# Kernel optimization log

Hardware: AMD Instinct MI355X
Metric: run time of the kernel (lower is better)

The kernel has to match this reference:

```python
import jax, jax.numpy as jnp
import numpy as np

N_NODES = 50000
N_IN = 512
HIDDEN = 64
N_CLASSES = 40
N_EDGES = 800000


def setup_inputs() -> dict:
    key = jax.random.key(0)
    ks = jax.random.split(key, 8)
    x = jax.random.normal(ks[0], (N_NODES, N_IN), dtype=jnp.float32)
    edge_index = jax.random.randint(ks[1], (2, N_EDGES), 0, N_NODES, dtype=jnp.int64)
    s1 = 1.0 / np.sqrt(N_IN)
    s2 = 1.0 / np.sqrt(HIDDEN)
    W1 = jax.random.uniform(ks[2], (N_IN, HIDDEN), jnp.float32, -s1, s1)
    b1 = jax.random.uniform(ks[3], (HIDDEN,), jnp.float32, -s1, s1)
    W2 = jax.random.uniform(ks[4], (HIDDEN, HIDDEN), jnp.float32, -s2, s2)
    b2 = jax.random.uniform(ks[5], (HIDDEN,), jnp.float32, -s2, s2)
    Wo = jax.random.uniform(ks[6], (HIDDEN, N_CLASSES), jnp.float32, -s2, s2)
    bo = jax.random.uniform(ks[7], (N_CLASSES,), jnp.float32, -s2, s2)
    return {"x": x, "W1": W1, "b1": b1, "W2": W2, "b2": b2,
            "Wo": Wo, "bo": bo, "edge_index": edge_index}


def _gcn_conv(x, W, b, row, col, n_nodes):
    # h = lin(x)
    h = x @ W + b
    # degree over row (with self loops already appended)
    deg = jnp.zeros((n_nodes,), dtype=h.dtype).at[row].add(1.0)
    dis = deg ** -0.5  # deg >= 1 thanks to self loops
    norm = dis[row] * dis[col]  # [E]
    # message: norm * x_j where x_j = h[row] (source); aggregate to col (target)
    msg = norm[:, None] * h[row]  # [E, d]
    return jax.ops.segment_sum(msg, col, num_segments=n_nodes)


def reference(x, W1, b1, W2, b2, Wo, bo, edge_index):
    n = x.shape[0]
    # add_self_loops
    loop = jnp.arange(n, dtype=edge_index.dtype)
    row = jnp.concatenate([edge_index[0], loop])
    col = jnp.concatenate([edge_index[1], loop])
    h = _gcn_conv(x, W1, b1, row, col, n)
    h = jax.nn.relu(h)
    # dropout is identity in eval mode (training=False)
    h = _gcn_conv(h, W2, b2, row, col, n)
    logits = h @ Wo + bo
    return jax.nn.log_softmax(logits, axis=1)
```

## Files before the change

### kernel.cpp

```cpp
#include <hip/hip_runtime.h>
#include <hip/hip_fp16.h>
#include <cstdint>

#define N_NODES   50000
#define N_IN      512
#define HIDDEN    64
#define N_CLASSES 40
#define N_EDGES   800000

#define G_BLOCKS  200
#define EPB       4000
#define NBINS     196
#define SCAN_N    (NBINS * G_BLOCKS)
#define SCAN_NB   ((SCAN_N + 1023) / 1024)
#define FOLD_N    (N_IN * 64 + 64 * 64 + 64)
#define FOLD_B    ((FOLD_N + 255) / 256)
#define GEMM1_B   ((N_NODES + 63) / 64)

#define OFF_HA    0u
#define OFF_HB    6400000u
#define OFF_DIS   12800000u
#define OFF_OFFS  13000000u
#define OFF_HISTC 13200016u
#define OFF_HISTR 13356816u
#define OFF_BSUM  13513616u
#define OFF_COLS  13514128u
#define OFF_ROWS  16714128u
#define OFF_EPACK 19914128u
#define OFF_W1T   23114128u
#define OFF_W2OT  23179664u
#define OFF_B2O   23187856u

typedef __attribute__((ext_vector_type(8))) short short8_t;
typedef __attribute__((ext_vector_type(4))) float f32x4;

__device__ __forceinline__ ushort f2bf(float f) {
    uint u = __float_as_uint(f);
    uint r = (u + 0x7FFFu + ((u >> 16) & 1u)) >> 16;
    return (ushort)r;
}
__device__ __forceinline__ float bf2f(ushort h) {
    return __uint_as_float((uint)h << 16);
}

__global__ __launch_bounds__(256) void hist_fold(const int* __restrict__ erow,
                                                 const int* __restrict__ ecol,
                                                 int* __restrict__ histC,
                                                 int* __restrict__ histR,
                                                 const float* __restrict__ W1,
                                                 const float* __restrict__ W2,
                                                 const float* __restrict__ Wo,
                                                 const float* __restrict__ b2,
                                                 ushort* __restrict__ w1t,
                                                 ushort* __restrict__ w2ot,
                                                 float* __restrict__ b2o) {
    __shared__ int hc[NBINS], hr[NBINS];
    int t = threadIdx.x;
    if (blockIdx.x < G_BLOCKS) {
        int b = blockIdx.x;
        if (t < NBINS) { hc[t] = 0; hr[t] = 0; }
        __syncthreads();
        int s = b * EPB;
        for (int i = s + t; i < s + EPB; i += 256) {
            atomicAdd(&hc[ecol[i] >> 8], 1);
            atomicAdd(&hr[erow[i] >> 8], 1);
        }
        __syncthreads();
        if (t < NBINS) {
            histC[t * G_BLOCKS + b] = hc[t];
            histR[t * G_BLOCKS + b] = hr[t];
        }
    } else {
        int i = (blockIdx.x - G_BLOCKS) * 256 + t;
        if (i < N_IN * 64) {
            int k = i >> 6, n = i & 63;
            w1t[n * N_IN + k] = f2bf(W1[i]);
        } else if (i < N_IN * 64 + 64 * 64) {
            int j = i - N_IN * 64;
            int k = j >> 6, n = j & 63;
            float v = 0.f;
            if (n < N_CLASSES)
                for (int jj = 0; jj < HIDDEN; jj++)
                    v += W2[k * HIDDEN + jj] * Wo[jj * N_CLASSES + n];
            w2ot[n * HIDDEN + k] = f2bf(v);
        } else if (i < FOLD_N) {
            int c = i - N_IN * 64 - 64 * 64;
            float v = 0.f;
            if (c < N_CLASSES)
                for (int jj = 0; jj < HIDDEN; jj++)
                    v += b2[jj] * Wo[jj * N_CLASSES + c];
            b2o[c] = v;
        }
    }
}

__global__ __launch_bounds__(256) void scan1(int* __restrict__ histC,
                                             int* __restrict__ histR,
                                             int* __restrict__ bsum, int n) {
    int* a  = blockIdx.y ? histR : histC;
    int* bs = bsum + blockIdx.y * 64;
    int t = threadIdx.x;
    int g = blockIdx.x * 1024 + t * 4;
    int v[4];
#pragma unroll
    for (int i = 0; i < 4; i++) v[i] = (g + i < n) ? a[g + i] : 0;
    int s = v[0] + v[1] + v[2] + v[3];
    int lane = t & 63, wid = t >> 6;
    int x = s;
#pragma unroll
    for (int d = 1; d < 64; d <<= 1) {
        int y = __shfl_up(x, d);
        if (lane >= d) x += y;
    }
    __shared__ int wt[4];
    if (lane == 63) wt[wid] = x;
    __syncthreads();
    int wo = 0;
    for (int w = 0; w < wid; w++) wo += wt[w];
    int run = wo + x - s;
#pragma unroll
    for (int i = 0; i < 4; i++) {
        if (g + i < n) a[g + i] = run;
        run += v[i];
    }
    if (t == 255) bs[blockIdx.x] = wo + x;
}

__global__ void scan2(int* bsum, int nb) {
    int* bs = bsum + blockIdx.x * 64;
    int lane = threadIdx.x;
    int v = (lane < nb) ? bs[lane] : 0;
    int x = v;
#pragma unroll
    for (int d = 1; d < 64; d <<= 1) {
        int y = __shfl_up(x, d);
        if (lane >= d) x += y;
    }
    if (lane < nb) bs[lane] = x - v;
}

__global__ __launch_bounds__(256) void scan3(int* __restrict__ histC,
                                             int* __restrict__ histR,
                                             const int* __restrict__ bsum, int n) {
    int* a = blockIdx.y ? histR : histC;
    const int* bs = bsum + blockIdx.y * 64;
    int i = blockIdx.x * 256 + threadIdx.x;
    if (i < n) a[i] += bs[i >> 10];
}

__global__ __launch_bounds__(256) void scatter_k(const int* __restrict__ erow,
                                                 const int* __restrict__ ecol,
                                                 const int* __restrict__ scC,
                                                 const int* __restrict__ scR,
                                                 uint* __restrict__ colSorted,
                                                 int* __restrict__ rowSorted) {
    __shared__ int curC[NBINS], curR[NBINS];
    int t = threadIdx.x, b = blockIdx.x;
    if (t < NBINS) {
        curC[t] = scC[t * G_BLOCKS + b];
        curR[t] = scR[t * G_BLOCKS + b];
    }
    __syncthreads();
    int s = b * EPB;
    for (int i = s + t; i < s + EPB; i += 256) {
        int r = erow[i], c = ecol[i];
        int p = atomicAdd(&curC[c >> 8], 1);
        colSorted[p] = (uint)r | ((uint)c << 16);
        int q = atomicAdd(&curR[r >> 8], 1);
        rowSorted[q] = r;
    }
}

__global__ __launch_bounds__(256) void fine_row(const int* __restrict__ rowSorted,
                                                const int* __restrict__ scR,
                                                float* __restrict__ disv) {
    __shared__ int cnt[256];
    int bin = blockIdx.x, t = threadIdx.x;
    int base = scR[bin * G_BLOCKS];
    int end  = (bin == NBINS - 1) ? N_EDGES : scR[(bin + 1) * G_BLOCKS];
    cnt[t] = 0;
    __syncthreads();
    for (int i = base + t; i < end; i += 256)
        atomicAdd(&cnt[rowSorted[i] & 255], 1);
    __syncthreads();
    int node = bin * 256 + t;
    if (node < N_NODES) disv[node] = rsqrtf((float)(cnt[t] + 1));
}

__global__ __launch_bounds__(256) void fine_col(const uint* __restrict__ colSorted,
                                                const int* __restrict__ scC,
                                                const float* __restrict__ disv,
                                                int* __restrict__ offs,
                                                uint* __restrict__ epack) {
    __shared__ int cnt[256];
    __shared__ int excl[256];
    __shared__ int wt[4];
    __shared__ float dvs[256];
    int bin = blockIdx.x, t = threadIdx.x;
    int base = scC[bin * G_BLOCKS];
    int end  = (bin == NBINS - 1) ? N_EDGES : scC[(bin + 1) * G_BLOCKS];
    cnt[t] = 0;
    int node = bin * 256 + t;
    dvs[t] = (node < N_NODES) ? disv[node] : 0.f;
    __syncthreads();
    for (int i = base + t; i < end; i += 256)
        atomicAdd(&cnt[(colSorted[i] >> 16) & 255], 1);
    __syncthreads();
    int lane = t & 63, w = t >> 6;
    int v = cnt[t];
    int x = v;
#pragma unroll
    for (int d = 1; d < 64; d <<= 1) {
        int y = __shfl_up(x, d);
        if (lane >= d) x += y;
    }
    if (lane == 63) wt[w] = x;
    __syncthreads();
    int wo = 0;
    for (int u = 0; u < w; u++) wo += wt[u];
    excl[t] = wo + x - v;
    cnt[t] = 0;
    if (node <= N_NODES) offs[node] = base + wo + x - v;
    __syncthreads();
    for (int i = base + t; i < end; i += 256) {
        uint pv = colSorted[i];
        int cl = (pv >> 16) & 255;
        int src = (int)(pv & 0xFFFFu);
        int p = base + excl[cl] + atomicAdd(&cnt[cl], 1);
        float nrm = disv[src] * dvs[cl];
        ushort nb_ = __half_as_ushort(__float2half_rn(nrm));
        epack[p] = ((uint)nb_ << 16) | (uint)src;
    }
}

template <bool ABF16>
__global__ __launch_bounds__(256) void gemm_mfma(const void* __restrict__ Av,
                                                 const ushort* __restrict__ WT,
                                                 const float* __restrict__ bias,
                                                 ushort* __restrict__ C,
                                                 int M, int K) {
    __shared__ ushort Asb[64][72];
    __shared__ ushort Bsb[64][72];
    int t = threadIdx.x;
    int w = t >> 6, lane = t & 63;
    int wm = w >> 1, wn = w & 1;
    int lr = lane & 15, lg = lane >> 4;
    int blockRow = blockIdx.x * 64;

    f32x4 acc[2][2];
#pragma unroll
    for (int i = 0; i < 2; i++)
#pragma unroll
        for (int j = 0; j < 2; j++) acc[i][j] = (f32x4){0.f, 0.f, 0.f, 0.f};

    for (int kk = 0; kk < K; kk += 64) {
#pragma unroll
        for (int u = 0; u < 2; u++) {
            int idx = t + u * 256;
            int m = idx >> 3;
            int k8 = (idx & 7) * 8;
            int row = blockRow + m;
            short8_t s;
            if (ABF16) {
                const ushort* A16 = (const ushort*)Av;
                if (row < M) s = *(const short8_t*)(A16 + (size_t)row * K + kk + k8);
                else s = (short8_t){0,0,0,0,0,0,0,0};
            } else {
                const float* A32 = (const float*)Av;
                float4 a0, a1;
                if (row < M) {
                    const float* p = A32 + (size_t)row * K + kk + k8;
                    a0 = *(const float4*)p;
                    a1 = *(const float4*)(p + 4);
                } else {
                    a0 = make_float4(0.f, 0.f, 0.f, 0.f);
                    a1 = a0;
                }
                s[0] = (short)f2bf(a0.x); s[1] = (short)f2bf(a0.y);
                s[2] = (short)f2bf(a0.z); s[3] = (short)f2bf(a0.w);
                s[4] = (short)f2bf(a1.x); s[5] = (short)f2bf(a1.y);
                s[6] = (short)f2bf(a1.z); s[7] = (short)f2bf(a1.w);
            }
            *(short8_t*)&Asb[m][k8] = s;
        }
#pragma unroll
        for (int u = 0; u < 2; u++) {
            int idx = t + u * 256;
            int n = idx >> 3;
            int k8 = (idx & 7) * 8;
            short8_t vv = *(const short8_t*)(WT + (size_t)n * K + kk + k8);
            *(short8_t*)&Bsb[n][k8] = vv;
        }
        __syncthreads();
#pragma unroll
        for (int ks = 0; ks < 2; ks++) {
            int k0 = ks * 32 + lg * 8;
            short8_t af[2], bf_[2];
#pragma unroll
            for (int mi = 0; mi < 2; mi++)
                af[mi] = *(const short8_t*)&Asb[wm * 32 + mi * 16 + lr][k0];
#pragma unroll
            for (int ni = 0; ni < 2; ni++)
                bf_[ni] = *(const short8_t*)&Bsb[wn * 32 + ni * 16 + lr][k0];
#pragma unroll
            for (int mi = 0; mi < 2; mi++)
#pragma unroll
                for (int ni = 0; ni < 2; ni++)
                    acc[mi][ni] = __builtin_amdgcn_mfma_f32_16x16x32_bf16(
                        af[mi], bf_[ni], acc[mi][ni], 0, 0, 0);
        }
        __syncthreads();
    }
#pragma unroll
    for (int mi = 0; mi < 2; mi++) {
#pragma unroll
        for (int ni = 0; ni < 2; ni++) {
            int col = wn * 32 + ni * 16 + lr;
            float bv = bias[col];
#pragma unroll
            for (int r = 0; r < 4; r++) {
                int row = blockRow + wm * 32 + mi * 16 + lg * 4 + r;
                if (row < M) C[(size_t)row * 64 + col] = f2bf(acc[mi][ni][r] + bv);
            }
        }
    }
}

template <int HEAD>
__global__ __launch_bounds__(256) void agg_v6(const ushort* __restrict__ H,
                                              const int* __restrict__ offs,
                                              const uint* __restrict__ epack,
                                              const float* __restrict__ disv,
                                              ushort* __restrict__ outH,
                                              const float* __restrict__ bo,
                                              float* __restrict__ outL) {
    int wv = (blockIdx.x * 256 + threadIdx.x) >> 6;
    int lane = threadIdx.x & 63;
    wv = __builtin_amdgcn_readfirstlane(wv);
    if (wv >= N_NODES) return;
    int s = offs[wv], e = offs[wv + 1];
    float dn = disv[wv];
    float acc = dn * dn * bf2f(H[(size_t)wv * 64 + lane]);

    for (int i = s; i < e; i += 16) {
        int cap = e - 1;
        uint ep[16];
#pragma unroll
        for (int u = 0; u < 16; u++)
            ep[u] = epack[min(i + u, cap)];
        float hv[16];
#pragma unroll
        for (int u = 0; u < 16; u++)
            hv[u] = bf2f(H[(size_t)(ep[u] & 0xFFFFu) * 64 + lane]);
#pragma unroll
        for (int u = 0; u < 16; u++) {
            uint wb = (i + u < e) ? (ep[u] >> 16) : 0u;
            float w = __half2float(__ushort_as_half((ushort)wb));
            acc = fmaf(w, hv[u], acc);
        }
    }

    if (!HEAD) {
        outH[(size_t)wv * 64 + lane] = f2bf(fmaxf(acc, 0.f));
    } else {
        float accL = (lane < N_CLASSES) ? acc + bo[lane] : -1e30f;
        float mx = accL;
#pragma unroll
        for (int d = 32; d; d >>= 1) mx = fmaxf(mx, __shfl_xor(mx, d));
        float ex = (lane < N_CLASSES) ? expf(accL - mx) : 0.f;
        float sm = ex;
#pragma unroll
        for (int d = 32; d; d >>= 1) sm += __shfl_xor(sm, d);
        if (lane < N_CLASSES)
            outL[(size_t)wv * N_CLASSES + lane] = accL - mx - logf(sm);
    }
}

extern "C" void kernel_launch(void* const* d_in, const int* in_sizes, int n_in,
                              void* d_out, int out_size, void* d_ws, size_t ws_size,
                              hipStream_t stream) {
    const float* x  = (const float*)d_in[0];
    const float* W1 = (const float*)d_in[1];
    const float* b1 = (const float*)d_in[2];
    const float* W2 = (const float*)d_in[3];
    const float* b2 = (const float*)d_in[4];
    const float* Wo = (const float*)d_in[5];
    const float* bo = (const float*)d_in[6];
    const int* ei   = (const int*)d_in[7];
    const int* erow = ei;
    const int* ecol = ei + N_EDGES;

    char* ws = (char*)d_ws;
    ushort* h_a   = (ushort*)(ws + OFF_HA);
    ushort* h_b   = (ushort*)(ws + OFF_HB);
    float* disv   = (float*)(ws + OFF_DIS);
    int*   offs   = (int*)(ws + OFF_OFFS);
    int*   histC  = (int*)(ws + OFF_HISTC);
    int*   histR  = (int*)(ws + OFF_HISTR);
    int*   bsum   = (int*)(ws + OFF_BSUM);
    uint*  colS   = (uint*)(ws + OFF_COLS);
    int*   rowS   = (int*)(ws + OFF_ROWS);
    uint*  epack  = (uint*)(ws + OFF_EPACK);
    ushort* w1t   = (ushort*)(ws + OFF_W1T);
    ushort* w2ot  = (ushort*)(ws + OFF_W2OT);
    float* b2o    = (float*)(ws + OFF_B2O);
    float* outp   = (float*)d_out;

    hist_fold<<<G_BLOCKS + FOLD_B, 256, 0, stream>>>(erow, ecol, histC, histR,
                                                     W1, W2, Wo, b2, w1t, w2ot, b2o);
    scan1<<<dim3(SCAN_NB, 2), 256, 0, stream>>>(histC, histR, bsum, SCAN_N);
    scan2<<<2, 64, 0, stream>>>(bsum, SCAN_NB);
    scan3<<<dim3((SCAN_N + 255) / 256, 2), 256, 0, stream>>>(histC, histR, bsum, SCAN_N);
    scatter_k<<<G_BLOCKS, 256, 0, stream>>>(erow, ecol, histC, histR, colS, rowS);
    fine_row<<<NBINS, 256, 0, stream>>>(rowS, histR, disv);
    fine_col<<<NBINS, 256, 0, stream>>>(colS, histC, disv, offs, epack);

    gemm_mfma<false><<<GEMM1_B, 256, 0, stream>>>(x, w1t, b1, h_a, N_NODES, N_IN);
    agg_v6<0><<<(N_NODES + 3) / 4, 256, 0, stream>>>(h_a, offs, epack, disv, h_b,
                                                     nullptr, nullptr);
    gemm_mfma<true><<<GEMM1_B, 256, 0, stream>>>(h_b, w2ot, b2o, h_a, N_NODES, HIDDEN);
    agg_v6<1><<<(N_NODES + 3) / 4, 256, 0, stream>>>(h_a, offs, epack, disv, nullptr,
                                                     bo, outp);
}
```

Measured before the change: 143.3 us.

## Split hidden features into two 32-column planes for cache-resident aggregation passes

The GEMMs now write their bf16 outputs as two separate planes of 32 features each instead of 64-wide rows. Each aggregation is split into two launches, one per plane, so the gathered working set per pass is halved (about 3.2 MB per plane) and is more likely to stay in cache. Each wave handles two edges at once with its half-waves and reduces them with a shuffle. This doubles the reads of the edge list and the aggregation launches, and the output head now needs a float partial buffer that is written in one pass and read in the next.

Measured after the change: 233.3 us. 1.63x slower.

```diff
diff --git a/kernel.cpp b/kernel.cpp
--- a/kernel.cpp
+++ b/kernel.cpp
@@ -16,6 +16,8 @@
 #define FOLD_N    (N_IN * 64 + 64 * 64 + 64)
 #define FOLD_B    ((FOLD_N + 255) / 256)
 #define GEMM1_B   ((N_NODES + 63) / 64)
+
+#define PLANE     ((size_t)N_NODES * 32)
 
 #define OFF_HA    0u
 #define OFF_HB    6400000u
@@ -30,6 +32,7 @@
 #define OFF_W1T   23114128u
 #define OFF_W2OT  23179664u
 #define OFF_B2O   23187856u
+#define OFF_PART  23188112u
 
 typedef __attribute__((ext_vector_type(8))) short short8_t;
 typedef __attribute__((ext_vector_type(4))) float f32x4;
@@ -263,7 +266,10 @@
             short8_t s;
             if (ABF16) {
                 const ushort* A16 = (const ushort*)Av;
-                if (row < M) s = *(const short8_t*)(A16 + (size_t)row * K + kk + k8);
+                int kk8 = kk + k8;
+                if (row < M)
+                    s = *(const short8_t*)(A16 + (size_t)(kk8 >> 5) * PLANE
+                                               + (size_t)row * 32 + (kk8 & 31));
                 else s = (short8_t){0,0,0,0,0,0,0,0};
             } else {
                 const float* A32 = (const float*)Av;
@@ -317,62 +323,72 @@
         for (int ni = 0; ni < 2; ni++) {
             int col = wn * 32 + ni * 16 + lr;
             float bv = bias[col];
+            ushort* Cp = C + (size_t)(col >> 5) * PLANE + (col & 31);
 #pragma unroll
             for (int r = 0; r < 4; r++) {
                 int row = blockRow + wm * 32 + mi * 16 + lg * 4 + r;
-                if (row < M) C[(size_t)row * 64 + col] = f2bf(acc[mi][ni][r] + bv);
+                if (row < M) Cp[(size_t)row * 32] = f2bf(acc[mi][ni][r] + bv);
             }
         }
     }
 }
 
-template <int HEAD>
-__global__ __launch_bounds__(256) void agg_v6(const ushort* __restrict__ H,
+template <int MODE>
+__global__ __launch_bounds__(256) void agg_pl(const ushort* __restrict__ Hp,
                                               const int* __restrict__ offs,
                                               const uint* __restrict__ epack,
                                               const float* __restrict__ disv,
-                                              ushort* __restrict__ outH,
+                                              ushort* __restrict__ outP,
+                                              float* __restrict__ part,
                                               const float* __restrict__ bo,
                                               float* __restrict__ outL) {
     int wv = (blockIdx.x * 256 + threadIdx.x) >> 6;
     int lane = threadIdx.x & 63;
     wv = __builtin_amdgcn_readfirstlane(wv);
     if (wv >= N_NODES) return;
+    int f = lane & 31, g = lane >> 5;
     int s = offs[wv], e = offs[wv + 1];
     float dn = disv[wv];
-    float acc = dn * dn * bf2f(H[(size_t)wv * 64 + lane]);
-
-    for (int i = s; i < e; i += 16) {
+    float selfv = bf2f(Hp[(size_t)wv * 32 + f]);
+    float acc = g ? 0.f : dn * dn * selfv;
+
+    for (int i = s; i < e; i += 8) {
         int cap = e - 1;
-        uint ep[16];
-#pragma unroll
-        for (int u = 0; u < 16; u++)
+        uint ep[8];
+#pragma unroll
+        for (int u = 0; u < 8; u++)
             ep[u] = epack[min(i + u, cap)];
-        float hv[16];
-#pragma unroll
-        for (int u = 0; u < 16; u++)
-            hv[u] = bf2f(H[(size_t)(ep[u] & 0xFFFFu) * 64 + lane]);
-#pragma unroll
-        for (int u = 0; u < 16; u++) {
-            uint wb = (i + u < e) ? (ep[u] >> 16) : 0u;
-            float w = __half2float(__ushort_as_half((ushort)wb));
-            acc = fmaf(w, hv[u], acc);
-        }
-    }
-
-    if (!HEAD) {
-        outH[(size_t)wv * 64 + lane] = f2bf(fmaxf(acc, 0.f));
+#pragma unroll
+        for (int u = 0; u < 4; u++) {
+            uint eg = g ? ep[2 * u + 1] : ep[2 * u];
+            int idx = i + 2 * u + g;
+            float hv = bf2f(Hp[(size_t)(eg & 0xFFFFu) * 32 + f]);
+            float w = (idx < e)
+                ? __half2float(__ushort_as_half((ushort)(eg >> 16))) : 0.f;
+            acc = fmaf(w, hv, acc);
+        }
+    }
+    acc += __shfl_xor(acc, 32);
+
+    if (MODE == 0) {
+        if (g == 0) outP[(size_t)wv * 32 + f] = f2bf(fmaxf(acc, 0.f));
+    } else if (MODE == 1) {
+        if (g == 0) part[(size_t)wv * 32 + f] = acc;
     } else {
-        float accL = (lane < N_CLASSES) ? acc + bo[lane] : -1e30f;
-        float mx = accL;
-#pragma unroll
-        for (int d = 32; d; d >>= 1) mx = fmaxf(mx, __shfl_xor(mx, d));
-        float ex = (lane < N_CLASSES) ? expf(accL - mx) : 0.f;
-        float sm = ex;
-#pragma unroll
-        for (int d = 32; d; d >>= 1) sm += __shfl_xor(sm, d);
-        if (lane < N_CLASSES)
-            outL[(size_t)wv * N_CLASSES + lane] = accL - mx - logf(sm);
+        float l0 = part[(size_t)wv * 32 + f] + bo[f];
+        bool v1 = (32 + f) < N_CLASSES;
+        float l1 = v1 ? acc + bo[32 + f] : -1e30f;
+        float mx = fmaxf(l0, l1);
+#pragma unroll
+        for (int d = 16; d; d >>= 1) mx = fmaxf(mx, __shfl_xor(mx, d));
+        float sm = expf(l0 - mx) + (v1 ? expf(l1 - mx) : 0.f);
+#pragma unroll
+        for (int d = 16; d; d >>= 1) sm += __shfl_xor(sm, d);
+        float ls = logf(sm);
+        if (g == 0) {
+            outL[(size_t)wv * N_CLASSES + f] = l0 - mx - ls;
+            if (v1) outL[(size_t)wv * N_CLASSES + 32 + f] = l1 - mx - ls;
+        }
     }
 }
 
@@ -404,7 +420,10 @@
     ushort* w1t   = (ushort*)(ws + OFF_W1T);
     ushort* w2ot  = (ushort*)(ws + OFF_W2OT);
     float* b2o    = (float*)(ws + OFF_B2O);
+    float* part   = (float*)(ws + OFF_PART);
     float* outp   = (float*)d_out;
+
+    int aggB = (N_NODES + 3) / 4;
 
     hist_fold<<<G_BLOCKS + FOLD_B, 256, 0, stream>>>(erow, ecol, histC, histR,
                                                      W1, W2, Wo, b2, w1t, w2ot, b2o);
@@ -416,9 +435,13 @@
     fine_col<<<NBINS, 256, 0, stream>>>(colS, histC, disv, offs, epack);
 
     gemm_mfma<false><<<GEMM1_B, 256, 0, stream>>>(x, w1t, b1, h_a, N_NODES, N_IN);
-    agg_v6<0><<<(N_NODES + 3) / 4, 256, 0, stream>>>(h_a, offs, epack, disv, h_b,
-                                                     nullptr, nullptr);
+    agg_pl<0><<<aggB, 256, 0, stream>>>(h_a, offs, epack, disv, h_b,
+                                        nullptr, nullptr, nullptr);
+    agg_pl<0><<<aggB, 256, 0, stream>>>(h_a + PLANE, offs, epack, disv, h_b + PLANE,
+                                        nullptr, nullptr, nullptr);
     gemm_mfma<true><<<GEMM1_B, 256, 0, stream>>>(h_b, w2ot, b2o, h_a, N_NODES, HIDDEN);
-    agg_v6<1><<<(N_NODES + 3) / 4, 256, 0, stream>>>(h_a, offs, epack, disv, nullptr,
-                                                     bo, outp);
-}
+    agg_pl<1><<<aggB, 256, 0, stream>>>(h_a, offs, epack, disv, nullptr,
+                                        part, nullptr, nullptr);
+    agg_pl<2><<<aggB, 256, 0, stream>>>(h_a + PLANE, offs, epack, disv, nullptr,
+                                        part, bo, outp);
+}
```
